# Kernel tuning notes

Measured on AMD Instinct MI355X. Metric: run time of the kernel, lower is better.

The kernel has to match this reference:

```python
import jax, jax.numpy as jnp
import numpy as np

T, D, F, V = 16384, 1024, 2048, 4096


def _mlp(x, w1, w2):
    # residual ReLU MLP stand-in for a transformer stack (tokenwise)
    return x + jax.nn.relu(x @ w1) @ w2


def setup_inputs() -> dict:
    key = jax.random.key(0)
    ks = jax.random.split(key, 11)
    s1 = 1.0 / np.sqrt(D)
    s2 = 1.0 / np.sqrt(F)
    g = lambda k, shape, sc: jax.random.normal(k, shape, dtype=jnp.float32) * sc
    return {
        "inputs_embeds": g(ks[0], (T, D), 1.0),
        "enc_w1": g(ks[1], (D, F), s1),
        "enc_w2": g(ks[2], (F, D), s2),
        "back_w1": g(ks[3], (D, F), s1),
        "back_w2": g(ks[4], (F, D), s2),
        "dec_w1": g(ks[5], (D, F), s1),
        "dec_w2": g(ks[6], (F, D), s2),
        "sp_w": g(ks[7], (D, 1), s1),
        "sp_b": jnp.zeros((1,), jnp.float32),
        "pos_emb": g(ks[8], (T, D), 0.02),
        "lm_head": g(ks[9], (D, V), s1),
        "cu_seq_lens": jnp.array([0, 4096, 8192, 12288, 16384], dtype=jnp.int32),
    }


def reference(inputs_embeds, enc_w1, enc_w2, back_w1, back_w2, dec_w1, dec_w2,
              sp_w, sp_b, pos_emb, lm_head, cu_seq_lens):
    # --- encoder (3-layer stack stand-in) ---
    enc = _mlp(inputs_embeds, enc_w1, enc_w2)                 # [T, D]
    # --- token gate: sigmoid + threshold ---
    w = jax.nn.sigmoid(enc @ sp_w + sp_b)[:, 0]               # [T]
    mask = w >= 0.5                                           # keep mask (= ~zero_mask)
    mi = mask.astype(jnp.int32)
    # --- ragged re-pack: within-segment rank of kept tokens (new position ids) ---
    ecs = jnp.cumsum(mi) - mi                                 # exclusive cumsum of kept
    seg = jnp.searchsorted(cu_seq_lens[1:], jnp.arange(T), side="right")
    base = ecs[cu_seq_lens[:-1]][seg]                         # kept-count before each segment
    new_pos = ecs - base                                      # arange(length) per new segment
    # stable sort places kept tokens first in original (packed) order,
    # exactly matching the per-segment concat of the torch version
    order = jnp.argsort(jnp.logical_not(mask), stable=True)   # [T]
    valid = mask[order]
    # gather + weight by gate value, add new position embedding
    gathered = (enc * w[:, None])[order] + pos_emb[new_pos[order]]
    gathered = jnp.where(valid[:, None], gathered, 0.0)
    # --- backbone compute on packed kept tokens ---
    bb = _mlp(gathered, back_w1, back_w2)                     # [T, D] (padded tail unused)
    # --- scatter-combine: kept slots <- backbone, dropped slots <- encoder residual ---
    inv = jnp.argsort(order)
    combined = jnp.where(mask[:, None], bb[inv], enc)         # [T, D]
    # --- decoder (3-layer stack stand-in) + lm head ---
    dec = _mlp(combined, dec_w1, dec_w2)
    logits = dec @ lm_head                                    # [T, V] fp32
    return logits
```

## Files before the change

kernel.cpp:

```cpp
#include <hip/hip_runtime.h>
#include <hip/hip_bf16.h>
#include <math.h>
#include <string.h>

static constexpr int TT = 16384;
static constexpr int DD = 1024;
static constexpr int FF = 2048;
static constexpr int VV = 4096;
static constexpr int CAP = 1024;
#define TAU 0.02f

using bf16 = __hip_bfloat16;
typedef __attribute__((ext_vector_type(8))) short bf16x8;
typedef __attribute__((ext_vector_type(4))) float f32x4;

__device__ inline void gload16(const void* g, void* l) {
    __builtin_amdgcn_global_load_lds(
        (const __attribute__((address_space(1))) void*)g,
        (__attribute__((address_space(3))) void*)l, 16, 0, 0);
}
__device__ inline float b2f(short s) {
    unsigned u = (unsigned)(unsigned short)s << 16;
    float f; __builtin_memcpy(&f, &u, 4); return f;
}
__device__ inline short f2b(float f) {
    bf16 h = __float2bfloat16(f);
    unsigned short us; __builtin_memcpy(&us, &h, 2); return (short)us;
}

template<int EPI, bool WB16, bool WF32, bool ROWLIM, bool GPART>
__global__ __launch_bounds__(512, 2)
void mgemm8(const bf16* __restrict__ A, const bf16* __restrict__ BT,
            const bf16* __restrict__ Xh,
            bf16* __restrict__ Ob, float* __restrict__ Of,
            float* __restrict__ gpart, const float* __restrict__ qv,
            int M, int N, int K, const int* __restrict__ rowlim)
{
    if constexpr (ROWLIM) { if ((int)blockIdx.y * 256 >= *rowlim) return; }
    const int m0 = blockIdx.y * 256, n0 = blockIdx.x * 256;

    extern __shared__ char smem[];

    const int tid = threadIdx.x;
    const int wv = tid >> 6, ln = tid & 63;
    const int wm = wv >> 2, wn = wv & 3;
    const int lr = ln & 15, lk = ln >> 4;
    const int swz = (lr & 7) << 4;

    const bf16* Ag = A  + (size_t)m0 * K;
    const bf16* Bg = BT + (size_t)n0 * K;

    const int NT = K >> 6;
    const int NI = NT >> 1;

    const int aoff0 = (wm * 128 + lr) * 128;
    const int boff0 = 32768 + (wn * 64 + lr) * 128;
    const int cb0 = (lk * 16) ^ swz;
    const int cb1 = (64 + lk * 16) ^ swz;

    auto STAGE = [&](const bf16* g, int h, int kt, int buf, int op) {
        const int r = ln >> 3;
        const int c = ((ln & 7) ^ r) * 8;
        const bf16* s = g + (size_t)(h * 128 + wv * 16 + r) * K + kt * 64 + c;
        char* d = smem + buf * 65536 + op * 32768 + h * 16384 + wv * 2048;
        gload16(s, d);
        gload16(s + (size_t)8 * K, d + 1024);
    };
    auto stage_j = [&](int j) {
        const int tile = j >> 2;
        if (tile >= NT) return;
        const int part = j & 3;
        const int buf = tile & 1;
        if (part < 2) STAGE(Bg, part, tile, buf, 1);
        else          STAGE(Ag, part - 2, tile, buf, 0);
    };

    bf16x8 afr[2][2], bfr[4][2];
    f32x4 acc[8][4];
    #pragma unroll
    for (int m = 0; m < 8; ++m)
        #pragma unroll
        for (int n = 0; n < 4; ++n) acc[m][n] = (f32x4){0.f, 0.f, 0.f, 0.f};

#define DS_A(BUF, Q) do {                                                     \
    const char* _p = smem + (BUF) * 65536 + aoff0 + (Q) * 4096;               \
    afr[0][0] = *(const bf16x8*)(_p + cb0);                                   \
    afr[0][1] = *(const bf16x8*)(_p + cb1);                                   \
    afr[1][0] = *(const bf16x8*)(_p + 2048 + cb0);                            \
    afr[1][1] = *(const bf16x8*)(_p + 2048 + cb1);                            \
} while (0)

#define DS_B(BUF) do {                                                        \
    const char* _p = smem + (BUF) * 65536 + boff0;                            \
    _Pragma("unroll")                                                         \
    for (int nf = 0; nf < 4; ++nf) {                                          \
        bfr[nf][0] = *(const bf16x8*)(_p + nf * 2048 + cb0);                  \
        bfr[nf][1] = *(const bf16x8*)(_p + nf * 2048 + cb1);                  \
    }                                                                         \
} while (0)

#define MFMAQ(Q) do {                                                         \
    __builtin_amdgcn_s_setprio(1);                                            \
    _Pragma("unroll")                                                         \
    for (int m2 = 0; m2 < 2; ++m2)                                            \
        _Pragma("unroll")                                                     \
        for (int nf = 0; nf < 4; ++nf) {                                      \
            acc[(Q) * 2 + m2][nf] = __builtin_amdgcn_mfma_f32_16x16x32_bf16(  \
                afr[m2][0], bfr[nf][0], acc[(Q) * 2 + m2][nf], 0, 0, 0);      \
            acc[(Q) * 2 + m2][nf] = __builtin_amdgcn_mfma_f32_16x16x32_bf16(  \
                afr[m2][1], bfr[nf][1], acc[(Q) * 2 + m2][nf], 0, 0, 0);      \
        }                                                                     \
    __builtin_amdgcn_s_setprio(0);                                            \
} while (0)

#define PHASE(Q, BUF, DOB, J, W)                                              \
    {                                                                         \
        DS_A(BUF, Q);                                                         \
        if (DOB) DS_B(BUF);                                                   \
        stage_j(J);                                                           \
        if ((W) == 1)      asm volatile("s_waitcnt vmcnt(6)" ::: "memory");   \
        else if ((W) == 2) asm volatile("s_waitcnt vmcnt(0)" ::: "memory");   \
        __builtin_amdgcn_sched_barrier(0);                                    \
        __builtin_amdgcn_s_barrier();                                         \
        MFMAQ(Q);                                                             \
        __builtin_amdgcn_s_barrier();                                         \
    }

    STAGE(Bg, 0, 0, 0, 1); STAGE(Bg, 1, 0, 0, 1);
    STAGE(Ag, 0, 0, 0, 0); STAGE(Ag, 1, 0, 0, 0);
    asm volatile("s_waitcnt vmcnt(4)" ::: "memory");
    STAGE(Bg, 0, 1, 1, 1); STAGE(Bg, 1, 1, 1, 1);
    STAGE(Ag, 0, 1, 1, 0);
    asm volatile("s_waitcnt vmcnt(6)" ::: "memory");
    __builtin_amdgcn_sched_barrier(0);
    __builtin_amdgcn_s_barrier();

    for (int i = 0; i < NI; ++i) {
        const int jb = 7 + 8 * i;
        const bool last = (i + 1 == NI);
        PHASE(0, 0, true,  jb + 0, 0);
        PHASE(1, 0, false, jb + 1, 0);
        PHASE(2, 0, false, jb + 2, 0);
        PHASE(3, 0, false, jb + 3, last ? 2 : 1);
        PHASE(0, 1, true,  jb + 4, 0);
        PHASE(1, 1, false, jb + 5, 0);
        PHASE(2, 1, false, jb + 6, 0);
        PHASE(3, 1, false, jb + 7, last ? 0 : 1);
    }

#undef PHASE
#undef MFMAQ
#undef DS_B
#undef DS_A

    if constexpr (GPART) {
        float qvv[4];
        #pragma unroll
        for (int nf = 0; nf < 4; ++nf) qvv[nf] = qv[n0 + wn * 64 + nf * 16 + lr];
        #pragma unroll
        for (int mf = 0; mf < 8; ++mf)
            #pragma unroll
            for (int rr = 0; rr < 4; ++rr) {
                float s = 0.f;
                #pragma unroll
                for (int nf = 0; nf < 4; ++nf) s += fmaxf(acc[mf][nf][rr], 0.f) * qvv[nf];
                s += __shfl_xor(s, 1, 64); s += __shfl_xor(s, 2, 64);
                s += __shfl_xor(s, 4, 64); s += __shfl_xor(s, 8, 64);
                if (lr == 0)
                    gpart[(size_t)(blockIdx.x * 4 + wn) * M +
                          (m0 + wm * 128 + mf * 16 + lk * 4 + rr)] = s;
            }
    }

    #pragma unroll
    for (int mf = 0; mf < 8; ++mf)
        #pragma unroll
        for (int nf = 0; nf < 4; ++nf)
            #pragma unroll
            for (int rr = 0; rr < 4; ++rr) {
                const int row = m0 + wm * 128 + mf * 16 + lk * 4 + rr;
                const int col = n0 + wn * 64 + nf * 16 + lr;
                float v = acc[mf][nf][rr];
                if constexpr (EPI == 1) v = fmaxf(v, 0.f);
                if constexpr (EPI == 3) v += __bfloat162float(Xh[(size_t)row * N + col]);
                if constexpr (WB16) Ob[(size_t)row * N + col] = __float2bfloat16(v);
                if constexpr (WF32) Of[(size_t)row * N + col] = v;
            }
}

__global__ void wtrans_all(const float* __restrict__ e1, const float* __restrict__ e2,
                           const float* __restrict__ b1, const float* __restrict__ b2,
                           const float* __restrict__ d1, const float* __restrict__ d2,
                           const float* __restrict__ lm,
                           bf16* __restrict__ e1T, bf16* __restrict__ e2T,
                           bf16* __restrict__ b1T, bf16* __restrict__ b2T,
                           bf16* __restrict__ d1T, bf16* __restrict__ d2T,
                           bf16* __restrict__ lmT)
{
    int bid = blockIdx.x;
    const float* W; bf16* T; int R, C;
    if (bid < 12288) {
        const int m = bid >> 11;
        bid &= 2047;
        R = (m & 1) ? FF : DD;
        C = (m & 1) ? DD : FF;
        switch (m) {
            case 0:  W = e1; T = e1T; break;
            case 1:  W = e2; T = e2T; break;
            case 2:  W = b1; T = b1T; break;
            case 3:  W = b2; T = b2T; break;
            case 4:  W = d1; T = d1T; break;
            default: W = d2; T = d2T; break;
        }
    } else {
        bid -= 12288; W = lm; T = lmT; R = DD; C = VV;
    }
    const int tc = C >> 5;
    const int cb = (bid % tc) * 32, rb = (bid / tc) * 32;

    __shared__ float tile[32][33];
    const int tx = threadIdx.x & 31, ty = threadIdx.x >> 5;
    #pragma unroll
    for (int i = 0; i < 32; i += 8)
        tile[ty + i][tx] = W[(size_t)(rb + ty + i) * C + cb + tx];
    __syncthreads();
    #pragma unroll
    for (int i = 0; i < 32; i += 8)
        T[(size_t)(cb + ty + i) * R + rb + tx] = __float2bfloat16(tile[tx][ty + i]);
}

__global__ void castx2(const float* __restrict__ x, const float* __restrict__ spw,
                       bf16* __restrict__ xb, float* __restrict__ sx)
{
    const int t  = blockIdx.x * 4 + (threadIdx.x >> 6);
    const int ln = threadIdx.x & 63;
    const float4* row = (const float4*)(x + (size_t)t * DD);
    const float4* sp4 = (const float4*)spw;
    bf16* dst = xb + (size_t)t * DD;
    float s = 0.f;
    #pragma unroll
    for (int q = 0; q < 4; ++q) {
        const int c = q * 64 + ln;
        const float4 v = row[c], p = sp4[c];
        s += v.x * p.x + v.y * p.y + v.z * p.z + v.w * p.w;
        dst[c * 4 + 0] = __float2bfloat16(v.x);
        dst[c * 4 + 1] = __float2bfloat16(v.y);
        dst[c * 4 + 2] = __float2bfloat16(v.z);
        dst[c * 4 + 3] = __float2bfloat16(v.w);
    }
    #pragma unroll
    for (int off = 32; off > 0; off >>= 1) s += __shfl_xor(s, off, 64);
    if (ln == 0) sx[t] = s;
}

__global__ void qvec(const float* __restrict__ w2, const float* __restrict__ sp,
                     float* __restrict__ q)
{
    const int f  = blockIdx.x * 4 + (threadIdx.x >> 6);
    const int ln = threadIdx.x & 63;
    float s = 0.f;
    const float* row = w2 + (size_t)f * DD;
    for (int k = ln; k < DD; k += 64) s += row[k] * sp[k];
    #pragma unroll
    for (int off = 32; off > 0; off >>= 1) s += __shfl_xor(s, off, 64);
    if (ln == 0) q[f] = s;
}

__global__ void gate2(const float* __restrict__ sx, const float* __restrict__ spb,
                      const float* __restrict__ gpart, float* __restrict__ w,
                      int* __restrict__ mi, int* __restrict__ flags,
                      int* __restrict__ cnt)
{
    const int t = blockIdx.x * 256 + threadIdx.x;
    float s = sx[t] + spb[0];
    #pragma unroll
    for (int j = 0; j < 32; ++j) s += gpart[(size_t)j * TT + t];
    const float sg = 1.f / (1.f + expf(-s));
    w[t]  = sg;
    mi[t] = (sg >= 0.5f) ? 1 : 0;
    if (fabsf(s) < TAU) {
        const int i = atomicAdd(cnt, 1);
        if (i < CAP) flags[i] = t;
    }
}

__global__ __launch_bounds__(256)
void fixh(const float* __restrict__ x, const float* __restrict__ w1,
          const int* __restrict__ flags, const int* __restrict__ cnt,
          float* __restrict__ Hpart)
{
    const int nb = min(*cnt, CAP);
    const int t0 = blockIdx.z * 32;
    if (t0 >= nb) return;
    const int ntk = min(32, nb - t0);
    const int f  = blockIdx.x * 256 + threadIdx.x;
    const int d0 = blockIdx.y * 256;

    __shared__ float xs[32][256];
    for (int i = threadIdx.x; i < 32 * 64; i += 256) {
        const int tk = i >> 6, dq = i & 63;
        float4 v = (tk < ntk)
            ? *(const float4*)&x[(size_t)flags[t0 + tk] * DD + d0 + dq * 4]
            : make_float4(0.f, 0.f, 0.f, 0.f);
        *(float4*)&xs[tk][dq * 4] = v;
    }
    __syncthreads();

    float acc[32];
    #pragma unroll
    for (int tk = 0; tk < 32; ++tk) acc[tk] = 0.f;
    for (int dd = 0; dd < 256; ++dd) {
        const float wv = w1[(size_t)(d0 + dd) * FF + f];
        #pragma unroll
        for (int tk = 0; tk < 32; ++tk) acc[tk] += xs[tk][dd] * wv;
    }
    for (int tk = 0; tk < ntk; ++tk)
        Hpart[((size_t)blockIdx.y * CAP + (t0 + tk)) * FF + f] = acc[tk];
}

__global__ void fixres2(const float* __restrict__ sx, const float* __restrict__ spb,
                        const float* __restrict__ Hpart, const float* __restrict__ qv,
                        const int* __restrict__ flags, const int* __restrict__ cnt,
                        float* __restrict__ w, int* __restrict__ mi)
{
    const int nb = min(*cnt, CAP);
    const int i  = blockIdx.x * 4 + (threadIdx.x >> 6);
    const int ln = threadIdx.x & 63;
    if (i >= nb) return;
    float s = 0.f;
    for (int f = ln; f < FF; f += 64) {
        const float h = Hpart[(size_t)(0 * CAP + i) * FF + f]
                      + Hpart[(size_t)(1 * CAP + i) * FF + f]
                      + Hpart[(size_t)(2 * CAP + i) * FF + f]
                      + Hpart[(size_t)(3 * CAP + i) * FF + f];
        s += fmaxf(h, 0.f) * qv[f];
    }
    #pragma unroll
    for (int off = 32; off > 0; off >>= 1) s += __shfl_xor(s, off, 64);
    if (ln == 0) {
        const int t = flags[i];
        const float logit = sx[t] + s + spb[0];
        const float sg = 1.f / (1.f + expf(-logit));
        w[t]  = sg;
        mi[t] = (sg >= 0.5f) ? 1 : 0;
    }
}

__global__ void scan_kernel(const int* __restrict__ mi, const int* __restrict__ cu,
                            int* __restrict__ ecs, int* __restrict__ meta)
{
    __shared__ int sums[256];
    const int tid  = threadIdx.x;
    const int base = tid * 64;
    int s = 0;
    for (int i = 0; i < 64; ++i) s += mi[base + i];
    sums[tid] = s;
    __syncthreads();
    for (int off = 1; off < 256; off <<= 1) {
        int v = (tid >= off) ? sums[tid - off] : 0;
        __syncthreads();
        sums[tid] += v;
        __syncthreads();
    }
    int run = (tid == 0) ? 0 : sums[tid - 1];
    for (int i = 0; i < 64; ++i) { ecs[base + i] = run; run += mi[base + i]; }
    if (tid == 255) meta[0] = sums[255];
    if (tid < 4) {
        const int idx = cu[tid];
        const int tc = idx >> 6, rem = idx & 63;
        int e = (tc == 0) ? 0 : sums[tc - 1];
        for (int i = 0; i < rem; ++i) e += mi[tc * 64 + i];
        meta[1 + tid] = e;
    }
}

__global__ void pack_kernel(const bf16* __restrict__ enc, const float* __restrict__ w,
                            const int* __restrict__ mi, const int* __restrict__ ecs,
                            const int* __restrict__ cu, const int* __restrict__ meta,
                            const float* __restrict__ pos_emb, bf16* __restrict__ Pb)
{
    const int t    = blockIdx.x * 4 + (threadIdx.x >> 6);
    const int lane = threadIdx.x & 63;
    if (!mi[t]) return;
    const int e = ecs[t];
    int seg = 0;
    #pragma unroll
    for (int ss = 1; ss < 4; ++ss) if (t >= cu[ss]) seg = ss;
    const int np = e - meta[1 + seg];
    const float wt = w[t];
    const bf16x8* src = (const bf16x8*)(enc + (size_t)t * DD);
    const float4* pe  = (const float4*)(pos_emb + (size_t)np * DD);
    bf16x8* dst = (bf16x8*)(Pb + (size_t)e * DD);
    #pragma unroll
    for (int q = 0; q < 2; ++q) {
        const int c = q * 64 + lane;
        const bf16x8 v = src[c];
        const float4 p0 = pe[c * 2], p1 = pe[c * 2 + 1];
        bf16x8 r;
        r[0] = f2b(b2f(v[0]) * wt + p0.x);
        r[1] = f2b(b2f(v[1]) * wt + p0.y);
        r[2] = f2b(b2f(v[2]) * wt + p0.z);
        r[3] = f2b(b2f(v[3]) * wt + p0.w);
        r[4] = f2b(b2f(v[4]) * wt + p1.x);
        r[5] = f2b(b2f(v[5]) * wt + p1.y);
        r[6] = f2b(b2f(v[6]) * wt + p1.z);
        r[7] = f2b(b2f(v[7]) * wt + p1.w);
        dst[c] = r;
    }
}

__global__ void combine_kernel(const bf16* __restrict__ ENCb, const bf16* __restrict__ BBb,
                               const int* __restrict__ mi, const int* __restrict__ ecs,
                               bf16* __restrict__ Cb)
{
    const int t    = blockIdx.x * 4 + (threadIdx.x >> 6);
    const int lane = threadIdx.x & 63;
    const bool kept = mi[t] != 0;
    const int4* src = kept ? (const int4*)(BBb + (size_t)ecs[t] * DD)
                           : (const int4*)(ENCb + (size_t)t * DD);
    int4* dst = (int4*)(Cb + (size_t)t * DD);
    #pragma unroll
    for (int q = 0; q < 2; ++q) dst[q * 64 + lane] = src[q * 64 + lane];
}

extern "C" void kernel_launch(void* const* d_in, const int* in_sizes, int n_in,
                              void* d_out, int out_size, void* d_ws, size_t ws_size,
                              hipStream_t stream)
{
    (void)in_sizes; (void)n_in; (void)out_size; (void)ws_size;
    const float* x   = (const float*)d_in[0];
    const float* ew1 = (const float*)d_in[1];
    const float* ew2 = (const float*)d_in[2];
    const float* bw1 = (const float*)d_in[3];
    const float* bw2 = (const float*)d_in[4];
    const float* dw1 = (const float*)d_in[5];
    const float* dw2 = (const float*)d_in[6];
    const float* spw = (const float*)d_in[7];
    const float* spb = (const float*)d_in[8];
    const float* pem = (const float*)d_in[9];
    const float* lmh = (const float*)d_in[10];
    const int*   cu  = (const int*)d_in[11];
    float* out = (float*)d_out;

    (void)hipFuncSetAttribute((const void*)mgemm8<1, true, false, false, true>,
                              hipFuncAttributeMaxDynamicSharedMemorySize, 131072);
    (void)hipFuncSetAttribute((const void*)mgemm8<3, true, false, false, false>,
                              hipFuncAttributeMaxDynamicSharedMemorySize, 131072);
    (void)hipFuncSetAttribute((const void*)mgemm8<1, true, false, true, false>,
                              hipFuncAttributeMaxDynamicSharedMemorySize, 131072);
    (void)hipFuncSetAttribute((const void*)mgemm8<3, true, false, true, false>,
                              hipFuncAttributeMaxDynamicSharedMemorySize, 131072);
    (void)hipFuncSetAttribute((const void*)mgemm8<1, true, false, false, false>,
                              hipFuncAttributeMaxDynamicSharedMemorySize, 131072);
    (void)hipFuncSetAttribute((const void*)mgemm8<0, false, true, false, false>,
                              hipFuncAttributeMaxDynamicSharedMemorySize, 131072);

    char* w = (char*)d_ws;
    auto alloc = [&](size_t bytes) { char* p = w; w += bytes; return p; };
    bf16* ew1T = (bf16*)alloc((size_t)FF * DD * 2);
    bf16* ew2T = (bf16*)alloc((size_t)DD * FF * 2);
    bf16* bw1T = (bf16*)alloc((size_t)FF * DD * 2);
    bf16* bw2T = (bf16*)alloc((size_t)DD * FF * 2);
    bf16* dw1T = (bf16*)alloc((size_t)FF * DD * 2);
    bf16* dw2T = (bf16*)alloc((size_t)DD * FF * 2);
    bf16* lmhT = (bf16*)alloc((size_t)VV * DD * 2);
    float* qv  = (float*)alloc((size_t)FF * 4);
    float* GP  = (float*)alloc((size_t)32 * TT * 4);
    float* WG  = (float*)alloc((size_t)TT * 4);
    int*  MI   = (int*)alloc((size_t)TT * 4);
    int*  ECS  = (int*)alloc((size_t)TT * 4);
    int*  META = (int*)alloc(64);
    float* SX  = (float*)alloc((size_t)TT * 4);
    int*  FLAGS= (int*)alloc((size_t)CAP * 4);
    int*  CNT  = (int*)alloc(64);
    bf16* Xb   = (bf16*)alloc((size_t)TT * DD * 2);
    bf16* Hb   = (bf16*)alloc((size_t)TT * FF * 2);
    bf16* ENCb = (bf16*)alloc((size_t)TT * DD * 2);
    bf16* Pb   = (bf16*)alloc((size_t)TT * DD * 2);
    bf16* BBb  = (bf16*)alloc((size_t)TT * DD * 2);
    bf16* Cb   = Xb;
    bf16* DECb = Pb;
    float* Hpart = (float*)BBb;

    const dim3 blk(256);
    const dim3 blk8(512);

    (void)hipMemsetAsync(CNT, 0, 4, stream);

    castx2<<<TT / 4, blk, 0, stream>>>(x, spw, Xb, SX);
    wtrans_all<<<16384, blk, 0, stream>>>(ew1, ew2, bw1, bw2, dw1, dw2, lmh,
                                          ew1T, ew2T, bw1T, bw2T, dw1T, dw2T, lmhT);
    qvec<<<FF / 4, blk, 0, stream>>>(ew2, spw, qv);

    mgemm8<1, true, false, false, true><<<dim3(FF / 256, TT / 256), blk8, 131072, stream>>>(
        Xb, ew1T, nullptr, Hb, nullptr, GP, qv, TT, FF, DD, nullptr);

    gate2<<<TT / 256, blk, 0, stream>>>(SX, spb, GP, WG, MI, FLAGS, CNT);
    fixh<<<dim3(FF / 256, 4, CAP / 32), blk, 0, stream>>>(x, ew1, FLAGS, CNT, Hpart);
    fixres2<<<CAP / 4, blk, 0, stream>>>(SX, spb, Hpart, qv, FLAGS, CNT, WG, MI);
    scan_kernel<<<1, blk, 0, stream>>>(MI, cu, ECS, META);

    mgemm8<3, true, false, false, false><<<dim3(DD / 256, TT / 256), blk8, 131072, stream>>>(
        Hb, ew2T, Xb, ENCb, nullptr, nullptr, nullptr, TT, DD, FF, nullptr);

    pack_kernel<<<TT / 4, blk, 0, stream>>>(ENCb, WG, MI, ECS, cu, META, pem, Pb);

    mgemm8<1, true, false, true, false><<<dim3(FF / 256, TT / 256), blk8, 131072, stream>>>(
        Pb, bw1T, nullptr, Hb, nullptr, nullptr, nullptr, TT, FF, DD, META);
    mgemm8<3, true, false, true, false><<<dim3(DD / 256, TT / 256), blk8, 131072, stream>>>(
        Hb, bw2T, Pb, BBb, nullptr, nullptr, nullptr, TT, DD, FF, META);

    combine_kernel<<<TT / 4, blk, 0, stream>>>(ENCb, BBb, MI, ECS, Cb);

    mgemm8<1, true, false, false, false><<<dim3(FF / 256, TT / 256), blk8, 131072, stream>>>(
        Cb, dw1T, nullptr, Hb, nullptr, nullptr, nullptr, TT, FF, DD, nullptr);
    mgemm8<3, true, false, false, false><<<dim3(DD / 256, TT / 256), blk8, 131072, stream>>>(
        Hb, dw2T, Cb, DECb, nullptr, nullptr, nullptr, TT, DD, FF, nullptr);

    mgemm8<0, false, true, false, false><<<dim3(VV / 256, TT / 256), blk8, 131072, stream>>>(
        DECb, lmhT, nullptr, nullptr, out, nullptr, nullptr, TT, VV, DD, nullptr);
}
```

Baseline: 705.5 us.

## Fuse pack and combine scatter into encoder and backbone GEMM epilogues

The encoder's second GEMM epilogue now writes kept rows straight into the packed backbone buffer, applying the gate weight and position embedding there. It writes dropped rows directly into the decoder input buffer. The backbone's second GEMM epilogue scatters its rows back to their original token positions, using a new inverse index that the scan kernel builds. This removes the separate pack and combine kernels and the ENCb/BBb intermediates, cutting launches and full-tensor round trips through memory. The cost is per-row index loads and non-contiguous scattered stores in the GEMM epilogues. The encoder output is also no longer rounded to bf16 before the gate scaling.

```diff
diff --git a/kernel.cpp b/kernel.cpp
--- a/kernel.cpp
+++ b/kernel.cpp
@@ -19,21 +19,26 @@
         (const __attribute__((address_space(1))) void*)g,
         (__attribute__((address_space(3))) void*)l, 16, 0, 0);
 }
-__device__ inline float b2f(short s) {
-    unsigned u = (unsigned)(unsigned short)s << 16;
-    float f; __builtin_memcpy(&f, &u, 4); return f;
-}
-__device__ inline short f2b(float f) {
-    bf16 h = __float2bfloat16(f);
-    unsigned short us; __builtin_memcpy(&us, &h, 2); return (short)us;
-}
-
-template<int EPI, bool WB16, bool WF32, bool ROWLIM, bool GPART>
+
+struct ScatArgs {
+    const float* w;
+    const int*   mi;
+    const int*   ecs;
+    const int*   it;
+    const int*   cu;
+    const int*   meta;
+    const float* pos;
+    bf16*        pb;
+    bf16*        cb;
+};
+
+template<int EPI, int WMODE, bool ROWLIM, bool GPART>
 __global__ __launch_bounds__(512, 2)
 void mgemm8(const bf16* __restrict__ A, const bf16* __restrict__ BT,
             const bf16* __restrict__ Xh,
             bf16* __restrict__ Ob, float* __restrict__ Of,
             float* __restrict__ gpart, const float* __restrict__ qv,
+            ScatArgs sa,
             int M, int N, int K, const int* __restrict__ rowlim)
 {
     if constexpr (ROWLIM) { if ((int)blockIdx.y * 256 >= *rowlim) return; }
@@ -172,20 +177,63 @@
             }
     }
 
+    int c1, c2, c3, kept;
+    if constexpr (WMODE == 2) { c1 = sa.cu[1]; c2 = sa.cu[2]; c3 = sa.cu[3]; }
+    if constexpr (WMODE == 3) { kept = sa.meta[0]; }
+
     #pragma unroll
     for (int mf = 0; mf < 8; ++mf)
         #pragma unroll
-        for (int nf = 0; nf < 4; ++nf)
-            #pragma unroll
-            for (int rr = 0; rr < 4; ++rr) {
-                const int row = m0 + wm * 128 + mf * 16 + lk * 4 + rr;
-                const int col = n0 + wn * 64 + nf * 16 + lr;
-                float v = acc[mf][nf][rr];
-                if constexpr (EPI == 1) v = fmaxf(v, 0.f);
-                if constexpr (EPI == 3) v += __bfloat162float(Xh[(size_t)row * N + col]);
-                if constexpr (WB16) Ob[(size_t)row * N + col] = __float2bfloat16(v);
-                if constexpr (WF32) Of[(size_t)row * N + col] = v;
+        for (int rr = 0; rr < 4; ++rr) {
+            const int row = m0 + wm * 128 + mf * 16 + lk * 4 + rr;
+
+            if constexpr (WMODE == 2) {
+                const int keep = sa.mi[row];
+                if (keep) {
+                    const int e = sa.ecs[row];
+                    const int seg = (row >= c1) + (row >= c2) + (row >= c3);
+                    const int np = e - sa.meta[1 + seg];
+                    const float wt = sa.w[row];
+                    #pragma unroll
+                    for (int nf = 0; nf < 4; ++nf) {
+                        const int col = n0 + wn * 64 + nf * 16 + lr;
+                        float v = acc[mf][nf][rr]
+                                + __bfloat162float(Xh[(size_t)row * N + col]);
+                        v = v * wt + sa.pos[(size_t)np * N + col];
+                        sa.pb[(size_t)e * N + col] = __float2bfloat16(v);
+                    }
+                } else {
+                    #pragma unroll
+                    for (int nf = 0; nf < 4; ++nf) {
+                        const int col = n0 + wn * 64 + nf * 16 + lr;
+                        float v = acc[mf][nf][rr]
+                                + __bfloat162float(Xh[(size_t)row * N + col]);
+                        sa.cb[(size_t)row * N + col] = __float2bfloat16(v);
+                    }
+                }
+            } else if constexpr (WMODE == 3) {
+                if (row < kept) {
+                    const int t = sa.it[row];
+                    #pragma unroll
+                    for (int nf = 0; nf < 4; ++nf) {
+                        const int col = n0 + wn * 64 + nf * 16 + lr;
+                        float v = acc[mf][nf][rr]
+                                + __bfloat162float(Xh[(size_t)row * N + col]);
+                        sa.cb[(size_t)t * N + col] = __float2bfloat16(v);
+                    }
+                }
+            } else {
+                #pragma unroll
+                for (int nf = 0; nf < 4; ++nf) {
+                    const int col = n0 + wn * 64 + nf * 16 + lr;
+                    float v = acc[mf][nf][rr];
+                    if constexpr (EPI == 1) v = fmaxf(v, 0.f);
+                    if constexpr (EPI == 3) v += __bfloat162float(Xh[(size_t)row * N + col]);
+                    if constexpr (WMODE == 1) Ob[(size_t)row * N + col] = __float2bfloat16(v);
+                    if constexpr (WMODE == 0) Of[(size_t)row * N + col] = v;
+                }
             }
+        }
 }
 
 __global__ void wtrans_all(const float* __restrict__ e1, const float* __restrict__ e2,
@@ -347,7 +395,8 @@
 }
 
 __global__ void scan_kernel(const int* __restrict__ mi, const int* __restrict__ cu,
-                            int* __restrict__ ecs, int* __restrict__ meta)
+                            int* __restrict__ ecs, int* __restrict__ it,
+                            int* __restrict__ meta)
 {
     __shared__ int sums[256];
     const int tid  = threadIdx.x;
@@ -363,7 +412,11 @@
         __syncthreads();
     }
     int run = (tid == 0) ? 0 : sums[tid - 1];
-    for (int i = 0; i < 64; ++i) { ecs[base + i] = run; run += mi[base + i]; }
+    for (int i = 0; i < 64; ++i) {
+        ecs[base + i] = run;
+        if (mi[base + i]) it[run] = base + i;
+        run += mi[base + i];
+    }
     if (tid == 255) meta[0] = sums[255];
     if (tid < 4) {
         const int idx = cu[tid];
@@ -372,55 +425,6 @@
         for (int i = 0; i < rem; ++i) e += mi[tc * 64 + i];
         meta[1 + tid] = e;
     }
-}
-
-__global__ void pack_kernel(const bf16* __restrict__ enc, const float* __restrict__ w,
-                            const int* __restrict__ mi, const int* __restrict__ ecs,
-                            const int* __restrict__ cu, const int* __restrict__ meta,
-                            const float* __restrict__ pos_emb, bf16* __restrict__ Pb)
-{
-    const int t    = blockIdx.x * 4 + (threadIdx.x >> 6);
-    const int lane = threadIdx.x & 63;
-    if (!mi[t]) return;
-    const int e = ecs[t];
-    int seg = 0;
-    #pragma unroll
-    for (int ss = 1; ss < 4; ++ss) if (t >= cu[ss]) seg = ss;
-    const int np = e - meta[1 + seg];
-    const float wt = w[t];
-    const bf16x8* src = (const bf16x8*)(enc + (size_t)t * DD);
-    const float4* pe  = (const float4*)(pos_emb + (size_t)np * DD);
-    bf16x8* dst = (bf16x8*)(Pb + (size_t)e * DD);
-    #pragma unroll
-    for (int q = 0; q < 2; ++q) {
-        const int c = q * 64 + lane;
-        const bf16x8 v = src[c];
-        const float4 p0 = pe[c * 2], p1 = pe[c * 2 + 1];
-        bf16x8 r;
-        r[0] = f2b(b2f(v[0]) * wt + p0.x);
-        r[1] = f2b(b2f(v[1]) * wt + p0.y);
-        r[2] = f2b(b2f(v[2]) * wt + p0.z);
-        r[3] = f2b(b2f(v[3]) * wt + p0.w);
-        r[4] = f2b(b2f(v[4]) * wt + p1.x);
-        r[5] = f2b(b2f(v[5]) * wt + p1.y);
-        r[6] = f2b(b2f(v[6]) * wt + p1.z);
-        r[7] = f2b(b2f(v[7]) * wt + p1.w);
-        dst[c] = r;
-    }
-}
-
-__global__ void combine_kernel(const bf16* __restrict__ ENCb, const bf16* __restrict__ BBb,
-                               const int* __restrict__ mi, const int* __restrict__ ecs,
-                               bf16* __restrict__ Cb)
-{
-    const int t    = blockIdx.x * 4 + (threadIdx.x >> 6);
-    const int lane = threadIdx.x & 63;
-    const bool kept = mi[t] != 0;
-    const int4* src = kept ? (const int4*)(BBb + (size_t)ecs[t] * DD)
-                           : (const int4*)(ENCb + (size_t)t * DD);
-    int4* dst = (int4*)(Cb + (size_t)t * DD);
-    #pragma unroll
-    for (int q = 0; q < 2; ++q) dst[q * 64 + lane] = src[q * 64 + lane];
 }
 
 extern "C" void kernel_launch(void* const* d_in, const int* in_sizes, int n_in,
@@ -442,17 +446,19 @@
     const int*   cu  = (const int*)d_in[11];
     float* out = (float*)d_out;
 
-    (void)hipFuncSetAttribute((const void*)mgemm8<1, true, false, false, true>,
-                              hipFuncAttributeMaxDynamicSharedMemorySize, 131072);
-    (void)hipFuncSetAttribute((const void*)mgemm8<3, true, false, false, false>,
-                              hipFuncAttributeMaxDynamicSharedMemorySize, 131072);
-    (void)hipFuncSetAttribute((const void*)mgemm8<1, true, false, true, false>,
-                              hipFuncAttributeMaxDynamicSharedMemorySize, 131072);
-    (void)hipFuncSetAttribute((const void*)mgemm8<3, true, false, true, false>,
-                              hipFuncAttributeMaxDynamicSharedMemorySize, 131072);
-    (void)hipFuncSetAttribute((const void*)mgemm8<1, true, false, false, false>,
-                              hipFuncAttributeMaxDynamicSharedMemorySize, 131072);
-    (void)hipFuncSetAttribute((const void*)mgemm8<0, false, true, false, false>,
+    (void)hipFuncSetAttribute((const void*)mgemm8<1, 1, false, true>,
+                              hipFuncAttributeMaxDynamicSharedMemorySize, 131072);
+    (void)hipFuncSetAttribute((const void*)mgemm8<3, 2, false, false>,
+                              hipFuncAttributeMaxDynamicSharedMemorySize, 131072);
+    (void)hipFuncSetAttribute((const void*)mgemm8<1, 1, true, false>,
+                              hipFuncAttributeMaxDynamicSharedMemorySize, 131072);
+    (void)hipFuncSetAttribute((const void*)mgemm8<3, 3, true, false>,
+                              hipFuncAttributeMaxDynamicSharedMemorySize, 131072);
+    (void)hipFuncSetAttribute((const void*)mgemm8<1, 1, false, false>,
+                              hipFuncAttributeMaxDynamicSharedMemorySize, 131072);
+    (void)hipFuncSetAttribute((const void*)mgemm8<3, 1, false, false>,
+                              hipFuncAttributeMaxDynamicSharedMemorySize, 131072);
+    (void)hipFuncSetAttribute((const void*)mgemm8<0, 0, false, false>,
                               hipFuncAttributeMaxDynamicSharedMemorySize, 131072);
 
     char* w = (char*)d_ws;
@@ -469,21 +475,24 @@
     float* WG  = (float*)alloc((size_t)TT * 4);
     int*  MI   = (int*)alloc((size_t)TT * 4);
     int*  ECS  = (int*)alloc((size_t)TT * 4);
+    int*  IT   = (int*)alloc((size_t)TT * 4);
     int*  META = (int*)alloc(64);
     float* SX  = (float*)alloc((size_t)TT * 4);
     int*  FLAGS= (int*)alloc((size_t)CAP * 4);
     int*  CNT  = (int*)alloc(64);
     bf16* Xb   = (bf16*)alloc((size_t)TT * DD * 2);
     bf16* Hb   = (bf16*)alloc((size_t)TT * FF * 2);
-    bf16* ENCb = (bf16*)alloc((size_t)TT * DD * 2);
     bf16* Pb   = (bf16*)alloc((size_t)TT * DD * 2);
-    bf16* BBb  = (bf16*)alloc((size_t)TT * DD * 2);
     bf16* Cb   = Xb;
     bf16* DECb = Pb;
-    float* Hpart = (float*)BBb;
+    float* Hpart = (float*)Pb;
 
     const dim3 blk(256);
     const dim3 blk8(512);
+
+    ScatArgs sa{WG, MI, ECS, IT, cu, META, pem, Pb, Cb};
+    ScatArgs sa0{nullptr, nullptr, nullptr, nullptr, nullptr, nullptr,
+                 nullptr, nullptr, nullptr};
 
     (void)hipMemsetAsync(CNT, 0, 4, stream);
 
@@ -492,31 +501,27 @@
                                           ew1T, ew2T, bw1T, bw2T, dw1T, dw2T, lmhT);
     qvec<<<FF / 4, blk, 0, stream>>>(ew2, spw, qv);
 
-    mgemm8<1, true, false, false, true><<<dim3(FF / 256, TT / 256), blk8, 131072, stream>>>(
-        Xb, ew1T, nullptr, Hb, nullptr, GP, qv, TT, FF, DD, nullptr);
+    mgemm8<1, 1, false, true><<<dim3(FF / 256, TT / 256), blk8, 131072, stream>>>(
+        Xb, ew1T, nullptr, Hb, nullptr, GP, qv, sa0, TT, FF, DD, nullptr);
 
     gate2<<<TT / 256, blk, 0, stream>>>(SX, spb, GP, WG, MI, FLAGS, CNT);
     fixh<<<dim3(FF / 256, 4, CAP / 32), blk, 0, stream>>>(x, ew1, FLAGS, CNT, Hpart);
     fixres2<<<CAP / 4, blk, 0, stream>>>(SX, spb, Hpart, qv, FLAGS, CNT, WG, MI);
-    scan_kernel<<<1, blk, 0, stream>>>(MI, cu, ECS, META);
-
-    mgemm8<3, true, false, false, false><<<dim3(DD / 256, TT / 256), blk8, 131072, stream>>>(
-        Hb, ew2T, Xb, ENCb, nullptr, nullptr, nullptr, TT, DD, FF, nullptr);
-
-    pack_kernel<<<TT / 4, blk, 0, stream>>>(ENCb, WG, MI, ECS, cu, META, pem, Pb);
-
-    mgemm8<1, true, false, true, false><<<dim3(FF / 256, TT / 256), blk8, 131072, stream>>>(
-        Pb, bw1T, nullptr, Hb, nullptr, nullptr, nullptr, TT, FF, DD, META);
-    mgemm8<3, true, false, true, false><<<dim3(DD / 256, TT / 256), blk8, 131072, stream>>>(
-        Hb, bw2T, Pb, BBb, nullptr, nullptr, nullptr, TT, DD, FF, META);
-
-    combine_kernel<<<TT / 4, blk, 0, stream>>>(ENCb, BBb, MI, ECS, Cb);
-
-    mgemm8<1, true, false, false, false><<<dim3(FF / 256, TT / 256), blk8, 131072, stream>>>(
-        Cb, dw1T, nullptr, Hb, nullptr, nullptr, nullptr, TT, FF, DD, nullptr);
-    mgemm8<3, true, false, false, false><<<dim3(DD / 256, TT / 256), blk8, 131072, stream>>>(
-        Hb, dw2T, Cb, DECb, nullptr, nullptr, nullptr, TT, DD, FF, nullptr);
-
-    mgemm8<0, false, true, false, false><<<dim3(VV / 256, TT / 256), blk8, 131072, stream>>>(
-        DECb, lmhT, nullptr, nullptr, out, nullptr, nullptr, TT, VV, DD, nullptr);
-}
+    scan_kernel<<<1, blk, 0, stream>>>(MI, cu, ECS, IT, META);
+
+    mgemm8<3, 2, false, false><<<dim3(DD / 256, TT / 256), blk8, 131072, stream>>>(
+        Hb, ew2T, Xb, nullptr, nullptr, nullptr, nullptr, sa, TT, DD, FF, nullptr);
+
+    mgemm8<1, 1, true, false><<<dim3(FF / 256, TT / 256), blk8, 131072, stream>>>(
+        Pb, bw1T, nullptr, Hb, nullptr, nullptr, nullptr, sa0, TT, FF, DD, META);
+    mgemm8<3, 3, true, false><<<dim3(DD / 256, TT / 256), blk8, 131072, stream>>>(
+        Hb, bw2T, Pb, nullptr, nullptr, nullptr, nullptr, sa, TT, DD, FF, META);
+
+    mgemm8<1, 1, false, false><<<dim3(FF / 256, TT / 256), blk8, 131072, stream>>>(
+        Cb, dw1T, nullptr, Hb, nullptr, nullptr, nullptr, sa0, TT, FF, DD, nullptr);
+    mgemm8<3, 1, false, false><<<dim3(DD / 256, TT / 256), blk8, 131072, stream>>>(
+        Hb, dw2T, Cb, DECb, nullptr, nullptr, nullptr, sa0, TT, DD, FF, nullptr);
+
+    mgemm8<0, 0, false, false><<<dim3(VV / 256, TT / 256), blk8, 131072, stream>>>(
+        DECb, lmhT, nullptr, nullptr, out, nullptr, nullptr, sa0, TT, VV, DD, nullptr);
+}
```

New measurement: 787.7 us. 11.6% more time.
